# Kernel optimization log

Measured on AMD Instinct MI355X. Metric: run time of the kernel, lower is better.

## Reference

```python
import jax, jax.numpy as jnp
import numpy as np

H = 256          # hidden_dim
E = 2 * H        # encoder output / attention embed dim = 512
MEL = 512        # mel_dim (must equal E for the original attention call to type-check)
NH = 8
HD = E // NH     # 64
B = 16
T = 128
V = 256          # vocab_size
NSPK = 100       # hardcoded speaker embedding rows
MAX_LEN = min(1000, T * 10)  # 1000 decode steps


def setup_inputs() -> dict:
    key = jax.random.key(0)
    ks = iter(jax.random.split(key, 40))

    def w(shape, s=0.05):
        return jax.random.normal(next(ks), shape, dtype=jnp.float32) * s

    return {
        'text_tokens': jax.random.randint(next(ks), (B, T), 0, V),
        'speaker_id': jax.random.randint(next(ks), (B,), 0, NSPK),
        'emb_text': w((V, H)),
        'emb_speaker': w((NSPK, H)),
        # bidirectional encoder LSTM (PyTorch gate order i,f,g,o)
        'enc_f_Wih': w((4 * H, H)), 'enc_f_Whh': w((4 * H, H)),
        'enc_f_bih': w((4 * H,)), 'enc_f_bhh': w((4 * H,)),
        'enc_b_Wih': w((4 * H, H)), 'enc_b_Whh': w((4 * H, H)),
        'enc_b_bih': w((4 * H,)), 'enc_b_bhh': w((4 * H,)),
        # multihead attention in/out projections
        'Wq': w((E, E)), 'bq': w((E,)),
        'Wk': w((E, E)), 'bk': w((E,)),
        'Wv': w((E, E)), 'bv': w((E,)),
        'Wo': w((E, E)), 'bo': w((E,)),
        # decoder LSTM (input dim = E + MEL); hidden state is re-zeroed every
        # step in the original (output state discarded), so Whh never acts.
        'dec_Wih': w((4 * H, E + MEL)), 'dec_Whh': w((4 * H, H)),
        'dec_bih': w((4 * H,)), 'dec_bhh': w((4 * H,)),
        'Wmel': w((MEL, H)), 'bmel': w((MEL,)),
        'Wstop': w((1, H)), 'bstop': w((1,)),
    }


def _lstm(x, Wih, Whh, bih, bhh, reverse=False):
    # x: [B, T, D] -> hidden sequence [B, T, H]
    Bx = x.shape[0]
    Hh = Whh.shape[1]
    h0 = jnp.zeros((Bx, Hh), x.dtype)

    def step(carry, xt):
        h, c = carry
        gates = xt @ Wih.T + bih + h @ Whh.T + bhh
        i, f, g, o = jnp.split(gates, 4, axis=-1)
        c = jax.nn.sigmoid(f) * c + jax.nn.sigmoid(i) * jnp.tanh(g)
        h = jax.nn.sigmoid(o) * jnp.tanh(c)
        return (h, c), h

    _, hs = jax.lax.scan(step, (h0, h0), jnp.swapaxes(x, 0, 1), reverse=reverse)
    return jnp.swapaxes(hs, 0, 1)


def reference(text_tokens, speaker_id, emb_text, emb_speaker,
              enc_f_Wih, enc_f_Whh, enc_f_bih, enc_f_bhh,
              enc_b_Wih, enc_b_Whh, enc_b_bih, enc_b_bhh,
              Wq, bq, Wk, bk, Wv, bv, Wo, bo,
              dec_Wih, dec_Whh, dec_bih, dec_bhh,
              Wmel, bmel, Wstop, bstop):
    # text + speaker embedding
    x = emb_text[text_tokens] + emb_speaker[speaker_id][:, None, :]   # [B,T,H]
    # bidirectional LSTM encoder
    enc_f = _lstm(x, enc_f_Wih, enc_f_Whh, enc_f_bih, enc_f_bhh)
    enc_b = _lstm(x, enc_b_Wih, enc_b_Whh, enc_b_bih, enc_b_bhh, reverse=True)
    enc = jnp.concatenate([enc_f, enc_b], axis=-1)                    # [B,T,E]

    # K/V projections are constant across decode steps -> hoist out of the loop
    K = (enc @ Wk.T + bk).reshape(B, T, NH, HD).transpose(0, 2, 1, 3)   # [B,NH,T,HD]
    Vv = (enc @ Wv.T + bv).reshape(B, T, NH, HD).transpose(0, 2, 1, 3)  # [B,NH,T,HD]
    scale = 1.0 / np.sqrt(HD).astype(np.float32)

    def step(mel_in, _):
        # single-query multihead attention (query = previous mel frame)
        q = (mel_in @ Wq.T + bq).reshape(B, NH, HD)                     # [B,NH,HD]
        w = jax.nn.softmax(jnp.einsum('bhd,bhtd->bht', q, K) * scale, axis=-1)
        ctx = jnp.einsum('bht,bhtd->bhd', w, Vv).reshape(B, E)
        attended = ctx @ Wo.T + bo                                      # [B,E]
        xin = jnp.concatenate([attended, mel_in], axis=-1)              # [B,E+MEL]
        # decoder LSTM single step from ZERO state each step (state discarded
        # in the original), so Whh term vanishes
        gates = xin @ dec_Wih.T + dec_bih + dec_bhh
        i, f, g, o = jnp.split(gates, 4, axis=-1)
        c = jax.nn.sigmoid(i) * jnp.tanh(g)
        h = jax.nn.sigmoid(o) * jnp.tanh(c)                             # [B,H]
        mel = h @ Wmel.T + bmel                                         # [B,MEL]
        stop = h @ Wstop.T + bstop                                      # [B,1]
        return mel, (mel, stop, w.mean(axis=1))

    mel0 = jnp.zeros((B, MEL), jnp.float32)
    _, (mels, stops, attns) = jax.lax.scan(step, mel0, None, length=MAX_LEN)

    mel_output = jnp.swapaxes(mels, 0, 1)    # [B,MAX_LEN,MEL]
    stop_output = jnp.swapaxes(stops, 0, 1)  # [B,MAX_LEN,1]
    attn_last = attns[-1][:, None, :]        # [B,1,T] (head-averaged, last step)
    return mel_output, stop_output, attn_last
```

## Files before the change

kernel.cpp:

```cpp
#include <hip/hip_runtime.h>
#include <hip/hip_bf16.h>


typedef unsigned short u16;
typedef unsigned int   u32;
#define DI __device__ __forceinline__

static constexpr size_t WS_BAR   = 0;
static constexpr size_t WS_GBUF  = 64*1024;
static constexpr size_t WS_HBUF  = 192*1024;
static constexpr size_t WS_PROBS = 208*1024;
static constexpr size_t WS_BIAS  = 272*1024;
static constexpr size_t WS_W2M   = 320*1024;
static constexpr size_t WS_WQH   = 832*1024;
static constexpr size_t WS_WCG   = 1344*1024;

static constexpr size_t OF_ENC_A = 262144;
static constexpr size_t OF_ENC_B = 1286144;
static constexpr size_t OF_XWF   = 4015744;
static constexpr size_t OF_XWB   = 6112896;

DI float bf2f(u16 u){ union{u32 i; float f;} v; v.i = ((u32)u)<<16; return v.f; }
DI u16 f2bf(float f){ union{float f; u32 i;} v; v.f = f;
  u32 r = v.i + 0x7fffu + ((v.i>>16)&1u); return (u16)(r>>16); }
DI float2 bf2x(u32 u){ union{u32 i; float f;} a,b; a.i = u<<16; b.i = u & 0xffff0000u;
  float2 r; r.x = a.f; r.y = b.f; return r; }
DI float dot8(uint4 wv, float4 a, float4 b){
  float2 w0 = bf2x(wv.x), w1 = bf2x(wv.y), w2 = bf2x(wv.z), w3 = bf2x(wv.w);
  return w0.x*a.x + w0.y*a.y + w1.x*a.z + w1.y*a.w
       + w2.x*b.x + w2.y*b.y + w3.x*b.z + w3.y*b.w;
}
DI float dot8f(float4 wa, float4 wb, float4 a, float4 b){
  return wa.x*a.x + wa.y*a.y + wa.z*a.z + wa.w*a.w
       + wb.x*b.x + wb.y*b.y + wb.z*b.z + wb.w*b.w;
}
DI float sigm(float x){ return 1.f/(1.f + __expf(-x)); }

DI float afload(const float* p){
  return __hip_atomic_load(p, __ATOMIC_RELAXED, __HIP_MEMORY_SCOPE_AGENT);
}
DI void afstore(float* p, float v){
  __hip_atomic_store(p, v, __ATOMIC_RELAXED, __HIP_MEMORY_SCOPE_AGENT);
}
DI void aadd(float* p, float v){
  __hip_atomic_fetch_add(p, v, __ATOMIC_RELAXED, __HIP_MEMORY_SCOPE_AGENT);
}

DI void bar_arrive(int* flags, int myidx, int t){
  __syncthreads();
  if (threadIdx.x == 0){
    __builtin_amdgcn_s_waitcnt(0);
    __hip_atomic_store(flags + myidx*32, t, __ATOMIC_RELAXED, __HIP_MEMORY_SCOPE_AGENT);
  }
}
DI void bar_wait(int* flags, int n, int t){
  if (threadIdx.x < 64){
    const int idx = threadIdx.x & (n-1);
    int v = __hip_atomic_load(flags + idx*32, __ATOMIC_RELAXED, __HIP_MEMORY_SCOPE_AGENT);
    while (__any(v < t)){
      __builtin_amdgcn_s_sleep(1);
      if (v < t)
        v = __hip_atomic_load(flags + idx*32, __ATOMIC_RELAXED, __HIP_MEMORY_SCOPE_AGENT);
    }
  }
  __asm__ __volatile__("" ::: "memory");
  __syncthreads();
}

__global__ __launch_bounds__(256) void k_init(int* bars, float* hbuf){
  const int i = blockIdx.x*256 + threadIdx.x;
  for (int k = i; k < 49152; k += 32*256) bars[k] = 0;
  if (i < 4096) hbuf[i] = 0.f;
}

__global__ __launch_bounds__(256) void k_xw(
    const int* __restrict__ tok, const int* __restrict__ spk,
    const float* __restrict__ et, const float* __restrict__ es,
    const float* __restrict__ WihF, const float* __restrict__ bihF, const float* __restrict__ bhhF,
    const float* __restrict__ WihB, const float* __restrict__ bihB, const float* __restrict__ bhhB,
    float* __restrict__ xwf, float* __restrict__ xwb){
  const int tid = threadIdx.x, bi = blockIdx.x;
  const int dir = bi & 1, jc = (bi >> 1) & 3, btg = bi >> 3;
  const int j = jc*256 + tid;
  const float* W = (dir ? WihB : WihF) + j*256;
  const float bias = (dir ? bihB : bihF)[j] + (dir ? bhhB : bhhF)[j];
  float* xw = dir ? xwb : xwf;

  __shared__ __align__(16) float lx[8][256];
  #pragma unroll
  for (int r = 0; r < 8; ++r){
    const int bt = btg*8 + r;
    lx[r][tid] = et[tok[bt]*256 + tid] + es[spk[bt>>7]*256 + tid];
  }
  __syncthreads();

  float acc[8];
  #pragma unroll
  for (int k2 = 0; k2 < 8; ++k2) acc[k2] = bias;
  for (int h = 0; h < 256; h += 8){
    float4 w0 = *(const float4*)(W + h);
    float4 w1 = *(const float4*)(W + h + 4);
    #pragma unroll
    for (int k2 = 0; k2 < 8; ++k2)
      acc[k2] += dot8f(w0, w1, *(const float4*)(&lx[k2][h]), *(const float4*)(&lx[k2][h+4]));
  }
  #pragma unroll
  for (int k2 = 0; k2 < 8; ++k2) xw[(btg*8 + k2)*1024 + j] = acc[k2];
}

__global__ __launch_bounds__(256) void k_fuse(
    const float* __restrict__ decW, const float* __restrict__ Wo,
    const float* __restrict__ Wmel, const float* __restrict__ Wq,
    u16* __restrict__ Wcg, u16* __restrict__ W2m, float* __restrict__ Wqh){
  const int tid = threadIdx.x, blk = blockIdx.x;
  float acc[4] = {0.f,0.f,0.f,0.f};
  if (blk < 512){
    const int g0 = (blk >> 1)*4, e = (blk & 1)*256 + tid;
    for (int jj = 0; jj < 512; ++jj){
      float wo = Wo[jj*512 + e];
      #pragma unroll
      for (int i2 = 0; i2 < 4; ++i2) acc[i2] += decW[(g0+i2)*1024 + jj] * wo;
    }
    #pragma unroll
    for (int i2 = 0; i2 < 4; ++i2) Wcg[(g0+i2)*512 + e] = f2bf(acc[i2]);
  } else if (blk < 768){
    const int g0 = (blk - 512)*4, h = tid;
    for (int m = 0; m < 512; ++m){
      float wm = Wmel[m*256 + h];
      #pragma unroll
      for (int i2 = 0; i2 < 4; ++i2) acc[i2] += decW[(g0+i2)*1024 + 512 + m] * wm;
    }
    #pragma unroll
    for (int i2 = 0; i2 < 4; ++i2) W2m[(g0+i2)*256 + h] = f2bf(acc[i2]);
  } else {
    const int j0 = (blk - 768)*4, h = tid;
    for (int e = 0; e < 512; ++e){
      float wm = Wmel[e*256 + h];
      #pragma unroll
      for (int i2 = 0; i2 < 4; ++i2) acc[i2] += Wq[(j0+i2)*512 + e] * wm;
    }
    #pragma unroll
    for (int i2 = 0; i2 < 4; ++i2) Wqh[(j0+i2)*256 + h] = acc[i2];
  }
}

__global__ __launch_bounds__(256) void k_bias(
    const float* __restrict__ Wq, const float* __restrict__ bq, const float* __restrict__ bmel,
    const float* __restrict__ decW, const float* __restrict__ bo,
    const float* __restrict__ bih, const float* __restrict__ bhh, float* __restrict__ biasws){
  const int o = blockIdx.x*256 + threadIdx.x;
  if (o < 512){
    float s = bq[o];
    for (int e = 0; e < 512; ++e) s += Wq[o*512 + e] * bmel[e];
    biasws[o] = s;
  } else {
    const int gr = o - 512;
    float s1 = bih[gr] + bhh[gr];
    for (int jj = 0; jj < 512; ++jj) s1 += decW[gr*1024 + jj] * bo[jj];
    biasws[512 + gr] = s1;
    float s2 = s1;
    for (int m = 0; m < 512; ++m) s2 += decW[gr*1024 + 512 + m] * bmel[m];
    biasws[1536 + gr] = s2;
  }
}

__global__ __launch_bounds__(128) void k_enc(
    const float* __restrict__ xwf, const float* __restrict__ xwb,
    const float* __restrict__ WhhF, const float* __restrict__ WhhB,
    float* encA, float* encB, int* bars){
  const int tid = threadIdx.x;
  const int xcd = blockIdx.x & 7, sl = blockIdx.x >> 3;
  const int grp = xcd*4 + (sl >> 3);
  const int w = sl & 7;
  const int dir = grp & 1, b = grp >> 1;
  int* bar = bars + (16 + grp)*1024;
  const float* Whh = dir ? WhhB : WhhF;
  const float* xw = dir ? xwb : xwf;
  float* encb = (b < 8 ? encA : encB) + (size_t)(b & 7)*65536;
  const int q = tid >> 5, ii = tid & 31;
  const int j = q*256 + w*32 + ii;
  const float* wr = Whh + j*256;

  __shared__ __align__(16) float l_h[256];
  __shared__ float l_g[4][32];
  __shared__ float l_c[32];
  if (tid < 32) l_c[tid] = 0.f;
  __syncthreads();

  for (int it = 0; it < 128; ++it){
    const int ts = dir ? (127 - it) : it;
    float acc = xw[(b*128 + ts)*1024 + j];
    if (it > 0){
      const int tp = dir ? (ts + 1) : (ts - 1);
      const float* hp = encb + tp*512 + dir*256;
      for (int i = tid; i < 256; i += 128) l_h[i] = afload(hp + i);
      __syncthreads();
      #pragma unroll 4
      for (int k = 0; k < 256; k += 8)
        acc += dot8f(*(const float4*)(wr + k), *(const float4*)(wr + k + 4),
                     *(const float4*)(&l_h[k]), *(const float4*)(&l_h[k + 4]));
    }
    l_g[q][ii] = acc;
    __syncthreads();
    if (tid < 32){
      float ig = l_g[0][tid], fg = l_g[1][tid], gg = l_g[2][tid], og = l_g[3][tid];
      float c = sigm(fg)*l_c[tid] + sigm(ig)*tanhf(gg);
      l_c[tid] = c;
      afstore(encb + ts*512 + dir*256 + w*32 + tid, sigm(og)*tanhf(c));
    }
    bar_arrive(bar, w, it+1);
    bar_wait(bar, 8, it+1);
  }
}

__global__ __launch_bounds__(256) void k_proj(
    const float* __restrict__ encA, const float* __restrict__ encB,
    const float* __restrict__ Wk, const float* __restrict__ bk,
    const float* __restrict__ Wv, const float* __restrict__ bv,
    float* outf){
  const int tid = threadIdx.x, x = blockIdx.x;
  const int role = x & 1, dc = (x >> 1) & 1, btg = x >> 2;
  const int row = dc*256 + tid;
  const float* W = (role ? Wv : Wk) + row*512;
  const float bias = (role ? bv : bk)[row];
  const int b = (btg*8) >> 7;
  const float* eb = (b < 8 ? encA : encB) + (size_t)(b & 7)*65536;
  float acc[8];
  #pragma unroll
  for (int k2 = 0; k2 < 8; ++k2) acc[k2] = bias;
  for (int e = 0; e < 512; e += 8){
    float4 wa = *(const float4*)(W + e);
    float4 wb = *(const float4*)(W + e + 4);
    #pragma unroll
    for (int k2 = 0; k2 < 8; ++k2){
      const float* ep = eb + ((btg*8 + k2) & 127)*512 + e;
      acc[k2] += dot8f(wa, wb, *(const float4*)(ep), *(const float4*)(ep + 4));
    }
  }
  const int head = row >> 6, dd = row & 63;
  float* kv = outf + (size_t)(b >> 1)*1024000 + (size_t)(b & 1)*131072;
  #pragma unroll
  for (int k2 = 0; k2 < 8; ++k2){
    const int ts = (btg*8 + k2) & 127;
    if (role == 0) kv[head*8192 + ts*64 + dd] = acc[k2];
    else           kv[65536 + head*8192 + dd*128 + ts] = acc[k2];
  }
}

__global__ __launch_bounds__(512) void k_decode(
    const float* __restrict__ Wqh,
    const u16*   __restrict__ Wcg,
    const u16*   __restrict__ W2m,
    const float* __restrict__ Wmel,
    const float* __restrict__ bmel,
    const float* __restrict__ Wstop, const float* __restrict__ bstop,
    const float* __restrict__ bq,
    const float* __restrict__ biasws,
    float* Gbuf,
    float* probs, int* bars,
    float* out){
  const int tid = threadIdx.x;
  const int b = blockIdx.x & 15, sidx = blockIdx.x >> 4;
  const int h = sidx >> 1, half = sidx & 1;
  const int d = tid & 63, ko = tid >> 6;
  int* bflag = bars + b*512;
  float* out_mel  = out;
  float* out_stop = out + 8192000;
  float* out_attn = out + 8208000;

  __shared__ __align__(16) float lK[128*68];
  __shared__ __align__(16) float lV[64*132];
  __shared__ __align__(16) float l_h[256];
  __shared__ __align__(16) float l_hw[8*36];
  __shared__ __align__(16) float l_q[64];
  __shared__ __align__(16) float l_p[128];
  __shared__ __align__(16) float l_ct[64];
  __shared__ __align__(16) float l_qt[8][64];
  __shared__ float l_r[2];

  const float* kv = out + (size_t)(b >> 1)*1024000 + (size_t)(b & 1)*131072;
  const int rg = tid >> 2, c4 = tid & 3;
  const int rw = tid >> 3, c8 = tid & 7;
  const int r2 = half*384 + h*48 + rw;

  {
    const float* gK = kv + h*8192;
    for (int i = tid; i < 2048; i += 512){
      const int r = i >> 4, c = i & 15;
      *(float4*)(lK + r*68 + c*4) = *(const float4*)(gK + r*64 + c*4);
    }
    const float* gV = kv + 65536 + h*8192;
    for (int i = tid; i < 2048; i += 512){
      const int r = i >> 5, c = i & 31;
      *(float4*)(lV + r*132 + c*4) = *(const float4*)(gV + r*128 + c*4);
    }
  }

  float4 wq[8];
  {
    const float* p = Wqh + (h*64 + d)*256 + ko*32;
    #pragma unroll
    for (int j = 0; j < 8; ++j) wq[j] = *(const float4*)(p + 4*j);
  }
  uint4 wcg[3][2];
  #pragma unroll
  for (int s = 0; s < 3; ++s){
    const int r = half*384 + rg*3 + s;
    const int orig = r + (r >= 256 ? 256 : 0);
    const u16* p = Wcg + orig*512 + h*64 + c4*16;
    wcg[s][0] = *(const uint4*)(p);
    wcg[s][1] = *(const uint4*)(p + 8);
  }
  uint4 w2[4];
  {
    const int orig2 = r2 + (r2 >= 256 ? 256 : 0);
    const u16* p = W2m + (tid < 384 ? orig2*256 + c8*32 : 0);
    #pragma unroll
    for (int j = 0; j < 4; ++j) w2[j] = *(const uint4*)(p + 8*j);
  }
  const float bq0 = bq[h*64 + d];
  const float bq1 = biasws[h*64 + d];
  const float bmd = bmel[h*64 + half*32 + ((tid & 255) >> 3)];
  float bgi0=0, bgg0=0, bgo0=0, bgi1=0, bgg1=0, bgo1=0;
  if (tid < 256){
    bgi0 = biasws[ 512 + tid]; bgg0 = biasws[1024 + tid]; bgo0 = biasws[1280 + tid];
    bgi1 = biasws[1536 + tid]; bgg1 = biasws[2048 + tid]; bgo1 = biasws[2304 + tid];
  }
  float4 wst4 = {0.f,0.f,0.f,0.f};
  if (h == 0 && half == 1 && tid < 64) wst4 = *(const float4*)(Wstop + tid*4);
  const float bst = bstop[0];

  if (tid < 256) l_h[tid] = 0.f;
  if (tid < 288) l_hw[tid] = 0.f;
  float hreg = 0.f;
  __syncthreads();

  int rot = 0;
  for (int t = 0; t < 1000; ++t){
    float* buf = Gbuf + (rot*16 + b)*768;
    {
      const float4* hh = (const float4*)(l_h + ko*32);
      l_qt[ko][d] = dot8f(wq[0], wq[1], hh[0], hh[1]) + dot8f(wq[2], wq[3], hh[2], hh[3])
                  + dot8f(wq[4], wq[5], hh[4], hh[5]) + dot8f(wq[6], wq[7], hh[6], hh[7]);
    }
    if (tid < 384){
      const float4* hh = (const float4*)(l_hw + c8*36);
      float w2p = dot8(w2[0], hh[0], hh[1]) + dot8(w2[1], hh[2], hh[3])
                + dot8(w2[2], hh[4], hh[5]) + dot8(w2[3], hh[6], hh[7]);
      w2p += __shfl_xor(w2p, 1);
      w2p += __shfl_xor(w2p, 2);
      w2p += __shfl_xor(w2p, 4);
      if (c8 == 0) aadd(buf + r2, w2p);
    } else if (t >= 2 && tid >= 432 && tid < 480){
      int rr = rot + 1; if (rr == 3) rr = 0;
      afstore(Gbuf + (rr*16 + b)*768 + sidx*48 + (tid - 432), 0.f);
    }
    __syncthreads();
    if (tid < 64){
      float qq = (t == 0 ? bq0 : bq1);
      #pragma unroll
      for (int k = 0; k < 8; ++k) qq += l_qt[k][tid];
      l_q[tid] = qq;
      __asm__ __volatile__("s_waitcnt lgkmcnt(0)" ::: "memory");
      const float* kr0 = lK + tid*68;
      const float* kr1 = lK + (tid + 64)*68;
      float s0 = 0.f, s1 = 0.f;
      #pragma unroll
      for (int k = 0; k < 64; k += 8){
        float4 qa = *(const float4*)(l_q + k), qb = *(const float4*)(l_q + k + 4);
        s0 += dot8f(*(const float4*)(kr0 + k), *(const float4*)(kr0 + k + 4), qa, qb);
        s1 += dot8f(*(const float4*)(kr1 + k), *(const float4*)(kr1 + k + 4), qa, qb);
      }
      s0 *= 0.125f; s1 *= 0.125f;
      float m = fmaxf(s0, s1);
      #pragma unroll
      for (int off = 32; off; off >>= 1) m = fmaxf(m, __shfl_xor(m, off));
      float p0 = __expf(s0 - m), p1 = __expf(s1 - m);
      float ss = p0 + p1;
      #pragma unroll
      for (int off = 32; off; off >>= 1) ss += __shfl_xor(ss, off);
      l_p[tid] = p0; l_p[tid + 64] = p1;
      __asm__ __volatile__("s_waitcnt lgkmcnt(0)" ::: "memory");
      const float* vr = lV + tid*132;
      float cs = 0.f;
      #pragma unroll
      for (int k = 0; k < 128; k += 8)
        cs += dot8f(*(const float4*)(vr + k), *(const float4*)(vr + k + 4),
                    *(const float4*)(l_p + k), *(const float4*)(l_p + k + 4));
      l_ct[tid] = cs / ss;
      if (tid == 0) l_r[0] = ss;
    }
    __syncthreads();
    {
      const float4* ct = (const float4*)(l_ct + c4*16);
      float4 c0 = ct[0], c1 = ct[1], c2 = ct[2], c3 = ct[3];
      float pr0 = dot8(wcg[0][0], c0, c1) + dot8(wcg[0][1], c2, c3);
      float pr1 = dot8(wcg[1][0], c0, c1) + dot8(wcg[1][1], c2, c3);
      float pr2 = dot8(wcg[2][0], c0, c1) + dot8(wcg[2][1], c2, c3);
      pr0 += __shfl_xor(pr0, 1); pr0 += __shfl_xor(pr0, 2);
      pr1 += __shfl_xor(pr1, 1); pr1 += __shfl_xor(pr1, 2);
      pr2 += __shfl_xor(pr2, 1); pr2 += __shfl_xor(pr2, 2);
      if (c4 == 0){
        const int rb = half*384 + rg*3;
        aadd(buf + rb,     pr0);
        aadd(buf + rb + 1, pr1);
        aadd(buf + rb + 2, pr2);
      }
    }
    bar_arrive(bflag, sidx, t+1);
    if (t == 1) bar_wait(bars + (b ^ 1)*512, 16, 1);
    if (t > 0){
      if (tid < 256){
        const int dd = half*32 + (tid >> 3), cc = tid & 7;
        const float* pm = Wmel + (h*64 + dd)*256 + cc*32;
        const float4* hh = (const float4*)(l_hw + cc*36);
        float mp = dot8f(*(const float4*)(pm),      *(const float4*)(pm + 4),  hh[0], hh[1])
                 + dot8f(*(const float4*)(pm + 8),  *(const float4*)(pm + 12), hh[2], hh[3])
                 + dot8f(*(const float4*)(pm + 16), *(const float4*)(pm + 20), hh[4], hh[5])
                 + dot8f(*(const float4*)(pm + 24), *(const float4*)(pm + 28), hh[6], hh[7]);
        mp += __shfl_xor(mp, 1); mp += __shfl_xor(mp, 2); mp += __shfl_xor(mp, 4);
        if (cc == 0) out_mel[((size_t)b*1000 + (t-1))*512 + h*64 + dd] = mp + bmd;
      }
      if (h == 0 && half == 1 && tid < 64){
        const float4 h4v = *(const float4*)(l_h + tid*4);
        float sp = wst4.x*h4v.x + wst4.y*h4v.y + wst4.z*h4v.z + wst4.w*h4v.w;
        #pragma unroll
        for (int off = 32; off; off >>= 1) sp += __shfl_xor(sp, off);
        if (tid == 0) out_stop[b*1000 + (t-1)] = sp + bst;
      }
    }
    bar_wait(bflag, 16, t+1);
    if (tid < 256){
      float gi = (t == 0 ? bgi0 : bgi1) + afload(buf + tid);
      float gg = (t == 0 ? bgg0 : bgg1) + afload(buf + 256 + tid);
      float go = (t == 0 ? bgo0 : bgo1) + afload(buf + 512 + tid);
      float c = sigm(gi) * tanhf(gg);
      hreg = sigm(go) * tanhf(c);
      l_h[tid] = hreg;
      l_hw[(tid >> 5)*36 + (tid & 31)] = hreg;
    }
    __syncthreads();
    rot = (rot == 2) ? 0 : rot + 1;
  }

  if (tid < 256){
    const int dd = half*32 + (tid >> 3), cc = tid & 7;
    const float* pm = Wmel + (h*64 + dd)*256 + cc*32;
    const float4* hh = (const float4*)(l_hw + cc*36);
    float mp = dot8f(*(const float4*)(pm),      *(const float4*)(pm + 4),  hh[0], hh[1])
             + dot8f(*(const float4*)(pm + 8),  *(const float4*)(pm + 12), hh[2], hh[3])
             + dot8f(*(const float4*)(pm + 16), *(const float4*)(pm + 20), hh[4], hh[5])
             + dot8f(*(const float4*)(pm + 24), *(const float4*)(pm + 28), hh[6], hh[7]);
    mp += __shfl_xor(mp, 1); mp += __shfl_xor(mp, 2); mp += __shfl_xor(mp, 4);
    if (cc == 0) out_mel[((size_t)b*1000 + 999)*512 + h*64 + dd] = mp + bmd;
  }
  if (h == 0 && half == 1 && tid < 64){
    const float4 h4v = *(const float4*)(l_h + tid*4);
    float sp = wst4.x*h4v.x + wst4.y*h4v.y + wst4.z*h4v.z + wst4.w*h4v.w;
    #pragma unroll
    for (int off = 32; off; off >>= 1) sp += __shfl_xor(sp, off);
    if (tid == 0) out_stop[b*1000 + 999] = sp + bst;
  }
  if (half == 0 && tid < 128)
    afstore(probs + (b*8 + h)*128 + tid, l_p[tid] / l_r[0]);
  bar_arrive(bflag, sidx, 1001);
  if (h == 0 && half == 0){
    bar_wait(bflag, 16, 1001);
    if (tid < 128){
      float ssum = 0.f;
      #pragma unroll
      for (int hh = 0; hh < 8; ++hh) ssum += afload(probs + (b*8 + hh)*128 + tid);
      out_attn[b*128 + tid] = ssum * 0.125f;
    }
  }
}

extern "C" void kernel_launch(void* const* d_in, const int* in_sizes, int n_in,
                              void* d_out, int out_size, void* d_ws, size_t ws_size,
                              hipStream_t stream){
  const int*   tok = (const int*)d_in[0];
  const int*   spk = (const int*)d_in[1];
  const float* emb_text = (const float*)d_in[2];
  const float* emb_spk  = (const float*)d_in[3];
  const float* WihF = (const float*)d_in[4];
  const float* WhhF = (const float*)d_in[5];
  const float* bihF = (const float*)d_in[6];
  const float* bhhF = (const float*)d_in[7];
  const float* WihB = (const float*)d_in[8];
  const float* WhhB = (const float*)d_in[9];
  const float* bihB = (const float*)d_in[10];
  const float* bhhB = (const float*)d_in[11];
  const float* Wq = (const float*)d_in[12];
  const float* bq = (const float*)d_in[13];
  const float* Wk = (const float*)d_in[14];
  const float* bk = (const float*)d_in[15];
  const float* Wv = (const float*)d_in[16];
  const float* bv = (const float*)d_in[17];
  const float* Wo = (const float*)d_in[18];
  const float* bo = (const float*)d_in[19];
  const float* decW = (const float*)d_in[20];
  const float* bih = (const float*)d_in[22];
  const float* bhh = (const float*)d_in[23];
  const float* Wmel = (const float*)d_in[24];
  const float* bmel = (const float*)d_in[25];
  const float* Wstop = (const float*)d_in[26];
  const float* bstop = (const float*)d_in[27];

  char* ws = (char*)d_ws;
  int*   bars   = (int*)(ws + WS_BAR);
  float* Gbuf   = (float*)(ws + WS_GBUF);
  float* hbuf   = (float*)(ws + WS_HBUF);
  float* probs  = (float*)(ws + WS_PROBS);
  float* biasws = (float*)(ws + WS_BIAS);
  u16*   W2m    = (u16*)(ws + WS_W2M);
  float* Wqh    = (float*)(ws + WS_WQH);
  u16*   Wcg    = (u16*)(ws + WS_WCG);

  float* outf = (float*)d_out;
  float* encA = outf + OF_ENC_A;
  float* encB = outf + OF_ENC_B;
  float* xwf  = outf + OF_XWF;
  float* xwb  = outf + OF_XWB;

  k_init <<<32,   256, 0, stream>>>(bars, hbuf);
  k_xw   <<<2048, 256, 0, stream>>>(tok, spk, emb_text, emb_spk,
                                    WihF, bihF, bhhF, WihB, bihB, bhhB, xwf, xwb);
  k_enc  <<<256,  128, 0, stream>>>(xwf, xwb, WhhF, WhhB, encA, encB, bars);
  k_fuse <<<896,  256, 0, stream>>>(decW, Wo, Wmel, Wq, Wcg, W2m, Wqh);
  k_bias <<<6,    256, 0, stream>>>(Wq, bq, bmel, decW, bo, bih, bhh, biasws);
  k_proj <<<1024, 256, 0, stream>>>(encA, encB, Wk, bk, Wv, bv, outf);
  k_decode<<<256, 512, 0, stream>>>(Wqh, Wcg, W2m, Wmel, bmel, Wstop, bstop,
                                    bq, biasws, Gbuf, probs, bars, outf);
}
```

Measured before the change: 6.617 ms.

## Interleave two batch elements per decode block to hide barrier latency

Each decode block now handles two batch elements (b0 and b0+8) with separate shared K/V, hidden and prob buffers, so the grid is halved to 128 blocks. Within each timestep the block does one element's work while the cross-block barrier for the other element completes, and the gate/LSTM update is moved to the start of the next step. Weights held in registers are reused across both elements. The cost is doubled shared memory per block, half as many blocks in flight, and twice the serial work per block per step.

New measurement: 12.39 ms. 1.87x slower.

```diff
diff --git a/kernel.cpp b/kernel.cpp
--- a/kernel.cpp
+++ b/kernel.cpp
@@ -260,39 +260,40 @@
     float* probs, int* bars,
     float* out){
   const int tid = threadIdx.x;
-  const int b = blockIdx.x & 15, sidx = blockIdx.x >> 4;
+  const int b0 = blockIdx.x & 7, sidx = blockIdx.x >> 3;
   const int h = sidx >> 1, half = sidx & 1;
   const int d = tid & 63, ko = tid >> 6;
-  int* bflag = bars + b*512;
   float* out_mel  = out;
   float* out_stop = out + 8192000;
   float* out_attn = out + 8208000;
 
-  __shared__ __align__(16) float lK[128*68];
-  __shared__ __align__(16) float lV[64*132];
-  __shared__ __align__(16) float l_h[256];
-  __shared__ __align__(16) float l_hw[8*36];
+  __shared__ __align__(16) float lK[2][128*68];
+  __shared__ __align__(16) float lV[2][64*132];
+  __shared__ __align__(16) float l_h[2][256];
+  __shared__ __align__(16) float l_hw[2][288];
   __shared__ __align__(16) float l_q[64];
-  __shared__ __align__(16) float l_p[128];
+  __shared__ __align__(16) float l_p[2][128];
   __shared__ __align__(16) float l_ct[64];
   __shared__ __align__(16) float l_qt[8][64];
   __shared__ float l_r[2];
 
-  const float* kv = out + (size_t)(b >> 1)*1024000 + (size_t)(b & 1)*131072;
   const int rg = tid >> 2, c4 = tid & 3;
   const int rw = tid >> 3, c8 = tid & 7;
   const int r2 = half*384 + h*48 + rw;
 
-  {
-    const float* gK = kv + h*8192;
+  #pragma unroll
+  for (int s = 0; s < 2; ++s){
+    const int bb = b0 + 8*s;
+    const float* kvs = out + (size_t)(bb >> 1)*1024000 + (size_t)(bb & 1)*131072;
+    const float* gK = kvs + h*8192;
     for (int i = tid; i < 2048; i += 512){
       const int r = i >> 4, c = i & 15;
-      *(float4*)(lK + r*68 + c*4) = *(const float4*)(gK + r*64 + c*4);
-    }
-    const float* gV = kv + 65536 + h*8192;
+      *(float4*)(&lK[s][r*68 + c*4]) = *(const float4*)(gK + r*64 + c*4);
+    }
+    const float* gV = kvs + 65536 + h*8192;
     for (int i = tid; i < 2048; i += 512){
       const int r = i >> 5, c = i & 31;
-      *(float4*)(lV + r*132 + c*4) = *(const float4*)(gV + r*128 + c*4);
+      *(float4*)(&lV[s][r*132 + c*4]) = *(const float4*)(gV + r*128 + c*4);
     }
   }
 
@@ -330,147 +331,187 @@
   if (h == 0 && half == 1 && tid < 64) wst4 = *(const float4*)(Wstop + tid*4);
   const float bst = bstop[0];
 
-  if (tid < 256) l_h[tid] = 0.f;
-  if (tid < 288) l_hw[tid] = 0.f;
-  float hreg = 0.f;
+  if (tid < 256){ l_h[0][tid] = 0.f; l_h[1][tid] = 0.f; }
+  if (tid < 288){ l_hw[0][tid] = 0.f; l_hw[1][tid] = 0.f; }
   __syncthreads();
 
-  int rot = 0;
   for (int t = 0; t < 1000; ++t){
-    float* buf = Gbuf + (rot*16 + b)*768;
-    {
-      const float4* hh = (const float4*)(l_h + ko*32);
-      l_qt[ko][d] = dot8f(wq[0], wq[1], hh[0], hh[1]) + dot8f(wq[2], wq[3], hh[2], hh[3])
-                  + dot8f(wq[4], wq[5], hh[4], hh[5]) + dot8f(wq[6], wq[7], hh[6], hh[7]);
-    }
-    if (tid < 384){
-      const float4* hh = (const float4*)(l_hw + c8*36);
-      float w2p = dot8(w2[0], hh[0], hh[1]) + dot8(w2[1], hh[2], hh[3])
-                + dot8(w2[2], hh[4], hh[5]) + dot8(w2[3], hh[6], hh[7]);
-      w2p += __shfl_xor(w2p, 1);
-      w2p += __shfl_xor(w2p, 2);
-      w2p += __shfl_xor(w2p, 4);
-      if (c8 == 0) aadd(buf + r2, w2p);
-    } else if (t >= 2 && tid >= 432 && tid < 480){
-      int rr = rot + 1; if (rr == 3) rr = 0;
-      afstore(Gbuf + (rr*16 + b)*768 + sidx*48 + (tid - 432), 0.f);
-    }
-    __syncthreads();
-    if (tid < 64){
-      float qq = (t == 0 ? bq0 : bq1);
-      #pragma unroll
-      for (int k = 0; k < 8; ++k) qq += l_qt[k][tid];
-      l_q[tid] = qq;
-      __asm__ __volatile__("s_waitcnt lgkmcnt(0)" ::: "memory");
-      const float* kr0 = lK + tid*68;
-      const float* kr1 = lK + (tid + 64)*68;
-      float s0 = 0.f, s1 = 0.f;
-      #pragma unroll
-      for (int k = 0; k < 64; k += 8){
-        float4 qa = *(const float4*)(l_q + k), qb = *(const float4*)(l_q + k + 4);
-        s0 += dot8f(*(const float4*)(kr0 + k), *(const float4*)(kr0 + k + 4), qa, qb);
-        s1 += dot8f(*(const float4*)(kr1 + k), *(const float4*)(kr1 + k + 4), qa, qb);
-      }
-      s0 *= 0.125f; s1 *= 0.125f;
-      float m = fmaxf(s0, s1);
-      #pragma unroll
-      for (int off = 32; off; off >>= 1) m = fmaxf(m, __shfl_xor(m, off));
-      float p0 = __expf(s0 - m), p1 = __expf(s1 - m);
-      float ss = p0 + p1;
-      #pragma unroll
-      for (int off = 32; off; off >>= 1) ss += __shfl_xor(ss, off);
-      l_p[tid] = p0; l_p[tid + 64] = p1;
-      __asm__ __volatile__("s_waitcnt lgkmcnt(0)" ::: "memory");
-      const float* vr = lV + tid*132;
-      float cs = 0.f;
-      #pragma unroll
-      for (int k = 0; k < 128; k += 8)
-        cs += dot8f(*(const float4*)(vr + k), *(const float4*)(vr + k + 4),
-                    *(const float4*)(l_p + k), *(const float4*)(l_p + k + 4));
-      l_ct[tid] = cs / ss;
-      if (tid == 0) l_r[0] = ss;
-    }
-    __syncthreads();
-    {
-      const float4* ct = (const float4*)(l_ct + c4*16);
-      float4 c0 = ct[0], c1 = ct[1], c2 = ct[2], c3 = ct[3];
-      float pr0 = dot8(wcg[0][0], c0, c1) + dot8(wcg[0][1], c2, c3);
-      float pr1 = dot8(wcg[1][0], c0, c1) + dot8(wcg[1][1], c2, c3);
-      float pr2 = dot8(wcg[2][0], c0, c1) + dot8(wcg[2][1], c2, c3);
-      pr0 += __shfl_xor(pr0, 1); pr0 += __shfl_xor(pr0, 2);
-      pr1 += __shfl_xor(pr1, 1); pr1 += __shfl_xor(pr1, 2);
-      pr2 += __shfl_xor(pr2, 1); pr2 += __shfl_xor(pr2, 2);
-      if (c4 == 0){
-        const int rb = half*384 + rg*3;
-        aadd(buf + rb,     pr0);
-        aadd(buf + rb + 1, pr1);
-        aadd(buf + rb + 2, pr2);
-      }
-    }
-    bar_arrive(bflag, sidx, t+1);
-    if (t == 1) bar_wait(bars + (b ^ 1)*512, 16, 1);
-    if (t > 0){
+    #pragma unroll
+    for (int s = 0; s < 2; ++s){
+      const int bb = b0 + 8*s;
+      int* bflag = bars + bb*512;
+      float* lHs  = l_h[s];
+      float* lHws = l_hw[s];
+      const float* lKs = lK[s];
+      const float* lVs = lV[s];
+      float* lPs = l_p[s];
+      if (t == 2) bar_wait(bars + (bb ^ 1)*512, 16, 1);
+      if (t >= 2){
+        if (tid < 256){
+          const int dd = half*32 + (tid >> 3), cc = tid & 7;
+          const float* pm = Wmel + (h*64 + dd)*256 + cc*32;
+          const float4* hh = (const float4*)(lHws + cc*36);
+          float mp = dot8f(*(const float4*)(pm),      *(const float4*)(pm + 4),  hh[0], hh[1])
+                   + dot8f(*(const float4*)(pm + 8),  *(const float4*)(pm + 12), hh[2], hh[3])
+                   + dot8f(*(const float4*)(pm + 16), *(const float4*)(pm + 20), hh[4], hh[5])
+                   + dot8f(*(const float4*)(pm + 24), *(const float4*)(pm + 28), hh[6], hh[7]);
+          mp += __shfl_xor(mp, 1); mp += __shfl_xor(mp, 2); mp += __shfl_xor(mp, 4);
+          if (cc == 0) out_mel[((size_t)bb*1000 + (t-2))*512 + h*64 + dd] = mp + bmd;
+        }
+        if (h == 0 && half == 1 && tid < 64){
+          const float4 h4v = *(const float4*)(lHs + tid*4);
+          float sp = wst4.x*h4v.x + wst4.y*h4v.y + wst4.z*h4v.z + wst4.w*h4v.w;
+          #pragma unroll
+          for (int off = 32; off; off >>= 1) sp += __shfl_xor(sp, off);
+          if (tid == 0) out_stop[bb*1000 + (t-2)] = sp + bst;
+        }
+      }
+      if (t >= 1){
+        bar_wait(bflag, 16, t);
+        const float* bufP = Gbuf + (((t-1)%3)*16 + bb)*768;
+        if (tid < 256){
+          float gi = (t == 1 ? bgi0 : bgi1) + afload(bufP + tid);
+          float gg = (t == 1 ? bgg0 : bgg1) + afload(bufP + 256 + tid);
+          float go = (t == 1 ? bgo0 : bgo1) + afload(bufP + 512 + tid);
+          float c = sigm(gi) * tanhf(gg);
+          float hv = sigm(go) * tanhf(c);
+          lHs[tid] = hv;
+          lHws[(tid >> 5)*36 + (tid & 31)] = hv;
+        }
+        __syncthreads();
+      }
+      float* buf = Gbuf + ((t%3)*16 + bb)*768;
+      {
+        const float4* hh = (const float4*)(lHs + ko*32);
+        l_qt[ko][d] = dot8f(wq[0], wq[1], hh[0], hh[1]) + dot8f(wq[2], wq[3], hh[2], hh[3])
+                    + dot8f(wq[4], wq[5], hh[4], hh[5]) + dot8f(wq[6], wq[7], hh[6], hh[7]);
+      }
+      if (tid < 384){
+        const float4* hh = (const float4*)(lHws + c8*36);
+        float w2p = dot8(w2[0], hh[0], hh[1]) + dot8(w2[1], hh[2], hh[3])
+                  + dot8(w2[2], hh[4], hh[5]) + dot8(w2[3], hh[6], hh[7]);
+        w2p += __shfl_xor(w2p, 1);
+        w2p += __shfl_xor(w2p, 2);
+        w2p += __shfl_xor(w2p, 4);
+        if (c8 == 0) aadd(buf + r2, w2p);
+      } else if (t >= 2 && tid >= 432 && tid < 480){
+        const int rr = (t+1)%3;
+        afstore(Gbuf + (rr*16 + bb)*768 + sidx*48 + (tid - 432), 0.f);
+      }
+      __syncthreads();
+      if (tid < 64){
+        float qq = (t == 0 ? bq0 : bq1);
+        #pragma unroll
+        for (int k = 0; k < 8; ++k) qq += l_qt[k][tid];
+        l_q[tid] = qq;
+        __asm__ __volatile__("s_waitcnt lgkmcnt(0)" ::: "memory");
+        const float* kr0 = lKs + tid*68;
+        const float* kr1 = lKs + (tid + 64)*68;
+        float s0 = 0.f, s1 = 0.f;
+        #pragma unroll
+        for (int k = 0; k < 64; k += 8){
+          float4 qa = *(const float4*)(l_q + k), qb = *(const float4*)(l_q + k + 4);
+          s0 += dot8f(*(const float4*)(kr0 + k), *(const float4*)(kr0 + k + 4), qa, qb);
+          s1 += dot8f(*(const float4*)(kr1 + k), *(const float4*)(kr1 + k + 4), qa, qb);
+        }
+        s0 *= 0.125f; s1 *= 0.125f;
+        float m = fmaxf(s0, s1);
+        #pragma unroll
+        for (int off = 32; off; off >>= 1) m = fmaxf(m, __shfl_xor(m, off));
+        float p0 = __expf(s0 - m), p1 = __expf(s1 - m);
+        float ss = p0 + p1;
+        #pragma unroll
+        for (int off = 32; off; off >>= 1) ss += __shfl_xor(ss, off);
+        lPs[tid] = p0; lPs[tid + 64] = p1;
+        __asm__ __volatile__("s_waitcnt lgkmcnt(0)" ::: "memory");
+        const float* vr = lVs + tid*132;
+        float cs = 0.f;
+        #pragma unroll
+        for (int k = 0; k < 128; k += 8)
+          cs += dot8f(*(const float4*)(vr + k), *(const float4*)(vr + k + 4),
+                      *(const float4*)(lPs + k), *(const float4*)(lPs + k + 4));
+        l_ct[tid] = cs / ss;
+        if (tid == 0) l_r[s] = ss;
+      }
+      __syncthreads();
+      {
+        const float4* ct = (const float4*)(l_ct + c4*16);
+        float4 c0 = ct[0], c1 = ct[1], c2 = ct[2], c3 = ct[3];
+        float pr0 = dot8(wcg[0][0], c0, c1) + dot8(wcg[0][1], c2, c3);
+        float pr1 = dot8(wcg[1][0], c0, c1) + dot8(wcg[1][1], c2, c3);
+        float pr2 = dot8(wcg[2][0], c0, c1) + dot8(wcg[2][1], c2, c3);
+        pr0 += __shfl_xor(pr0, 1); pr0 += __shfl_xor(pr0, 2);
+        pr1 += __shfl_xor(pr1, 1); pr1 += __shfl_xor(pr1, 2);
+        pr2 += __shfl_xor(pr2, 1); pr2 += __shfl_xor(pr2, 2);
+        if (c4 == 0){
+          const int rb = half*384 + rg*3;
+          aadd(buf + rb,     pr0);
+          aadd(buf + rb + 1, pr1);
+          aadd(buf + rb + 2, pr2);
+        }
+      }
+      bar_arrive(bflag, sidx, t+1);
+    }
+  }
+
+  #pragma unroll
+  for (int s = 0; s < 2; ++s){
+    const int bb = b0 + 8*s;
+    int* bflag = bars + bb*512;
+    float* lHs  = l_h[s];
+    float* lHws = l_hw[s];
+    float* lPs  = l_p[s];
+    #pragma unroll
+    for (int e = 0; e < 2; ++e){
+      const int tm = 998 + e;
+      if (e == 1){
+        bar_wait(bflag, 16, 1000);
+        const float* bufP = Gbuf + ((999%3)*16 + bb)*768;
+        if (tid < 256){
+          float gi = bgi1 + afload(bufP + tid);
+          float gg = bgg1 + afload(bufP + 256 + tid);
+          float go = bgo1 + afload(bufP + 512 + tid);
+          float c = sigm(gi) * tanhf(gg);
+          float hv = sigm(go) * tanhf(c);
+          lHs[tid] = hv;
+          lHws[(tid >> 5)*36 + (tid & 31)] = hv;
+        }
+        __syncthreads();
+      }
       if (tid < 256){
         const int dd = half*32 + (tid >> 3), cc = tid & 7;
         const float* pm = Wmel + (h*64 + dd)*256 + cc*32;
-        const float4* hh = (const float4*)(l_hw + cc*36);
+        const float4* hh = (const float4*)(lHws + cc*36);
         float mp = dot8f(*(const float4*)(pm),      *(const float4*)(pm + 4),  hh[0], hh[1])
                  + dot8f(*(const float4*)(pm + 8),  *(const float4*)(pm + 12), hh[2], hh[3])
                  + dot8f(*(const float4*)(pm + 16), *(const float4*)(pm + 20), hh[4], hh[5])
                  + dot8f(*(const float4*)(pm + 24), *(const float4*)(pm + 28), hh[6], hh[7]);
         mp += __shfl_xor(mp, 1); mp += __shfl_xor(mp, 2); mp += __shfl_xor(mp, 4);
-        if (cc == 0) out_mel[((size_t)b*1000 + (t-1))*512 + h*64 + dd] = mp + bmd;
+        if (cc == 0) out_mel[((size_t)bb*1000 + tm)*512 + h*64 + dd] = mp + bmd;
       }
       if (h == 0 && half == 1 && tid < 64){
-        const float4 h4v = *(const float4*)(l_h + tid*4);
+        const float4 h4v = *(const float4*)(lHs + tid*4);
         float sp = wst4.x*h4v.x + wst4.y*h4v.y + wst4.z*h4v.z + wst4.w*h4v.w;
         #pragma unroll
         for (int off = 32; off; off >>= 1) sp += __shfl_xor(sp, off);
-        if (tid == 0) out_stop[b*1000 + (t-1)] = sp + bst;
-      }
-    }
-    bar_wait(bflag, 16, t+1);
-    if (tid < 256){
-      float gi = (t == 0 ? bgi0 : bgi1) + afload(buf + tid);
-      float gg = (t == 0 ? bgg0 : bgg1) + afload(buf + 256 + tid);
-      float go = (t == 0 ? bgo0 : bgo1) + afload(buf + 512 + tid);
-      float c = sigm(gi) * tanhf(gg);
-      hreg = sigm(go) * tanhf(c);
-      l_h[tid] = hreg;
-      l_hw[(tid >> 5)*36 + (tid & 31)] = hreg;
-    }
-    __syncthreads();
-    rot = (rot == 2) ? 0 : rot + 1;
-  }
-
-  if (tid < 256){
-    const int dd = half*32 + (tid >> 3), cc = tid & 7;
-    const float* pm = Wmel + (h*64 + dd)*256 + cc*32;
-    const float4* hh = (const float4*)(l_hw + cc*36);
-    float mp = dot8f(*(const float4*)(pm),      *(const float4*)(pm + 4),  hh[0], hh[1])
-             + dot8f(*(const float4*)(pm + 8),  *(const float4*)(pm + 12), hh[2], hh[3])
-             + dot8f(*(const float4*)(pm + 16), *(const float4*)(pm + 20), hh[4], hh[5])
-             + dot8f(*(const float4*)(pm + 24), *(const float4*)(pm + 28), hh[6], hh[7]);
-    mp += __shfl_xor(mp, 1); mp += __shfl_xor(mp, 2); mp += __shfl_xor(mp, 4);
-    if (cc == 0) out_mel[((size_t)b*1000 + 999)*512 + h*64 + dd] = mp + bmd;
-  }
-  if (h == 0 && half == 1 && tid < 64){
-    const float4 h4v = *(const float4*)(l_h + tid*4);
-    float sp = wst4.x*h4v.x + wst4.y*h4v.y + wst4.z*h4v.z + wst4.w*h4v.w;
-    #pragma unroll
-    for (int off = 32; off; off >>= 1) sp += __shfl_xor(sp, off);
-    if (tid == 0) out_stop[b*1000 + 999] = sp + bst;
-  }
-  if (half == 0 && tid < 128)
-    afstore(probs + (b*8 + h)*128 + tid, l_p[tid] / l_r[0]);
-  bar_arrive(bflag, sidx, 1001);
-  if (h == 0 && half == 0){
-    bar_wait(bflag, 16, 1001);
-    if (tid < 128){
-      float ssum = 0.f;
-      #pragma unroll
-      for (int hh = 0; hh < 8; ++hh) ssum += afload(probs + (b*8 + hh)*128 + tid);
-      out_attn[b*128 + tid] = ssum * 0.125f;
+        if (tid == 0) out_stop[bb*1000 + tm] = sp + bst;
+      }
+    }
+    if (half == 0 && tid < 128)
+      afstore(probs + (bb*8 + h)*128 + tid, lPs[tid] / l_r[s]);
+    bar_arrive(bflag, sidx, 1001);
+  }
+  #pragma unroll
+  for (int s = 0; s < 2; ++s){
+    const int bb = b0 + 8*s;
+    if (h == 0 && half == 0){
+      bar_wait(bars + bb*512, 16, 1001);
+      if (tid < 128){
+        float ssum = 0.f;
+        #pragma unroll
+        for (int hh = 0; hh < 8; ++hh) ssum += afload(probs + (bb*8 + hh)*128 + tid);
+        out_attn[bb*128 + tid] = ssum * 0.125f;
+      }
     }
   }
 }
@@ -529,6 +570,6 @@
   k_fuse <<<896,  256, 0, stream>>>(decW, Wo, Wmel, Wq, Wcg, W2m, Wqh);
   k_bias <<<6,    256, 0, stream>>>(Wq, bq, bmel, decW, bo, bih, bhh, biasws);
   k_proj <<<1024, 256, 0, stream>>>(encA, encB, Wk, bk, Wv, bv, outf);
-  k_decode<<<256, 512, 0, stream>>>(Wqh, Wcg, W2m, Wmel, bmel, Wstop, bstop,
+  k_decode<<<128, 512, 0, stream>>>(Wqh, Wcg, W2m, Wmel, bmel, Wstop, bstop,
                                     bq, biasws, Gbuf, probs, bars, outf);
 }
```

## Double-buffer decoder hidden state and defer mel projection off the critical path

Applied to the files above, without the earlier changes.

Restructures the decode loop so each step starts by waiting on the barrier and computing h from the gate buffer. The mel/stop projection for step t-2 now runs between the barrier wait and the LSTM nonlinearity, using a double-buffered copy of the previous hidden state. The projection moves off the stretch between bar_arrive and bar_wait, and the loop tail's extra sync is folded into the loop head. It adds an epilogue for the last two steps plus more shared memory, and output writes now lag by two steps.

Measured after the change: 7.458 ms. +12.7%, slower.

```diff
diff --git a/kernel.cpp b/kernel.cpp
--- a/kernel.cpp
+++ b/kernel.cpp
@@ -264,14 +264,15 @@
   const int h = sidx >> 1, half = sidx & 1;
   const int d = tid & 63, ko = tid >> 6;
   int* bflag = bars + b*512;
+  int* pflag = bars + (b ^ 1)*512;
   float* out_mel  = out;
   float* out_stop = out + 8192000;
   float* out_attn = out + 8208000;
 
   __shared__ __align__(16) float lK[128*68];
   __shared__ __align__(16) float lV[64*132];
-  __shared__ __align__(16) float l_h[256];
-  __shared__ __align__(16) float l_hw[8*36];
+  __shared__ __align__(16) float l_h[2][256];
+  __shared__ __align__(16) float l_hw[2][288];
   __shared__ __align__(16) float l_q[64];
   __shared__ __align__(16) float l_p[128];
   __shared__ __align__(16) float l_ct[64];
@@ -330,21 +331,56 @@
   if (h == 0 && half == 1 && tid < 64) wst4 = *(const float4*)(Wstop + tid*4);
   const float bst = bstop[0];
 
-  if (tid < 256) l_h[tid] = 0.f;
-  if (tid < 288) l_hw[tid] = 0.f;
-  float hreg = 0.f;
+  if (tid < 256) l_h[0][tid] = 0.f;
+  if (tid < 288) l_hw[0][tid] = 0.f;
   __syncthreads();
 
-  int rot = 0;
   for (int t = 0; t < 1000; ++t){
-    float* buf = Gbuf + (rot*16 + b)*768;
+    const int cur = t & 1, prv = cur ^ 1;
+    if (t >= 1) bar_wait(bflag, 16, t);
+    if (t == 2) bar_wait(pflag, 16, 1);
+    float gi = 0.f, gg = 0.f, go = 0.f;
+    if (t >= 1 && tid < 256){
+      const float* bp = Gbuf + (((t-1)%3)*16 + b)*768;
+      gi = afload(bp + tid); gg = afload(bp + 256 + tid); go = afload(bp + 512 + tid);
+    }
+    if (t >= 2){
+      if (tid < 256){
+        const int dd = half*32 + (tid >> 3), cc = tid & 7;
+        const float* pm = Wmel + (h*64 + dd)*256 + cc*32;
+        const float4* hh = (const float4*)(&l_hw[prv][cc*36]);
+        float mp = dot8f(*(const float4*)(pm),      *(const float4*)(pm + 4),  hh[0], hh[1])
+                 + dot8f(*(const float4*)(pm + 8),  *(const float4*)(pm + 12), hh[2], hh[3])
+                 + dot8f(*(const float4*)(pm + 16), *(const float4*)(pm + 20), hh[4], hh[5])
+                 + dot8f(*(const float4*)(pm + 24), *(const float4*)(pm + 28), hh[6], hh[7]);
+        mp += __shfl_xor(mp, 1); mp += __shfl_xor(mp, 2); mp += __shfl_xor(mp, 4);
+        if (cc == 0) out_mel[((size_t)b*1000 + (t-2))*512 + h*64 + dd] = mp + bmd;
+      }
+      if (h == 0 && half == 1 && tid < 64){
+        const float4 h4v = *(const float4*)(&l_h[prv][tid*4]);
+        float sp = wst4.x*h4v.x + wst4.y*h4v.y + wst4.z*h4v.z + wst4.w*h4v.w;
+        #pragma unroll
+        for (int off = 32; off; off >>= 1) sp += __shfl_xor(sp, off);
+        if (tid == 0) out_stop[b*1000 + (t-2)] = sp + bst;
+      }
+    }
+    if (t >= 1 && tid < 256){
+      float gI = (t == 1 ? bgi0 : bgi1) + gi;
+      float gG = (t == 1 ? bgg0 : bgg1) + gg;
+      float gO = (t == 1 ? bgo0 : bgo1) + go;
+      float hv = sigm(gO) * tanhf(sigm(gI) * tanhf(gG));
+      l_h[cur][tid] = hv;
+      l_hw[cur][(tid >> 5)*36 + (tid & 31)] = hv;
+    }
+    __syncthreads();
+    float* buf = Gbuf + ((t%3)*16 + b)*768;
     {
-      const float4* hh = (const float4*)(l_h + ko*32);
+      const float4* hh = (const float4*)(&l_h[cur][ko*32]);
       l_qt[ko][d] = dot8f(wq[0], wq[1], hh[0], hh[1]) + dot8f(wq[2], wq[3], hh[2], hh[3])
                   + dot8f(wq[4], wq[5], hh[4], hh[5]) + dot8f(wq[6], wq[7], hh[6], hh[7]);
     }
     if (tid < 384){
-      const float4* hh = (const float4*)(l_hw + c8*36);
+      const float4* hh = (const float4*)(&l_hw[cur][c8*36]);
       float w2p = dot8(w2[0], hh[0], hh[1]) + dot8(w2[1], hh[2], hh[3])
                 + dot8(w2[2], hh[4], hh[5]) + dot8(w2[3], hh[6], hh[7]);
       w2p += __shfl_xor(w2p, 1);
@@ -352,7 +388,7 @@
       w2p += __shfl_xor(w2p, 4);
       if (c8 == 0) aadd(buf + r2, w2p);
     } else if (t >= 2 && tid >= 432 && tid < 480){
-      int rr = rot + 1; if (rr == 3) rr = 0;
+      const int rr = (t+1)%3;
       afstore(Gbuf + (rr*16 + b)*768 + sidx*48 + (tid - 432), 0.f);
     }
     __syncthreads();
@@ -408,45 +444,43 @@
       }
     }
     bar_arrive(bflag, sidx, t+1);
-    if (t == 1) bar_wait(bars + (b ^ 1)*512, 16, 1);
-    if (t > 0){
-      if (tid < 256){
-        const int dd = half*32 + (tid >> 3), cc = tid & 7;
-        const float* pm = Wmel + (h*64 + dd)*256 + cc*32;
-        const float4* hh = (const float4*)(l_hw + cc*36);
-        float mp = dot8f(*(const float4*)(pm),      *(const float4*)(pm + 4),  hh[0], hh[1])
-                 + dot8f(*(const float4*)(pm + 8),  *(const float4*)(pm + 12), hh[2], hh[3])
-                 + dot8f(*(const float4*)(pm + 16), *(const float4*)(pm + 20), hh[4], hh[5])
-                 + dot8f(*(const float4*)(pm + 24), *(const float4*)(pm + 28), hh[6], hh[7]);
-        mp += __shfl_xor(mp, 1); mp += __shfl_xor(mp, 2); mp += __shfl_xor(mp, 4);
-        if (cc == 0) out_mel[((size_t)b*1000 + (t-1))*512 + h*64 + dd] = mp + bmd;
-      }
-      if (h == 0 && half == 1 && tid < 64){
-        const float4 h4v = *(const float4*)(l_h + tid*4);
-        float sp = wst4.x*h4v.x + wst4.y*h4v.y + wst4.z*h4v.z + wst4.w*h4v.w;
-        #pragma unroll
-        for (int off = 32; off; off >>= 1) sp += __shfl_xor(sp, off);
-        if (tid == 0) out_stop[b*1000 + (t-1)] = sp + bst;
-      }
-    }
-    bar_wait(bflag, 16, t+1);
-    if (tid < 256){
-      float gi = (t == 0 ? bgi0 : bgi1) + afload(buf + tid);
-      float gg = (t == 0 ? bgg0 : bgg1) + afload(buf + 256 + tid);
-      float go = (t == 0 ? bgo0 : bgo1) + afload(buf + 512 + tid);
-      float c = sigm(gi) * tanhf(gg);
-      hreg = sigm(go) * tanhf(c);
-      l_h[tid] = hreg;
-      l_hw[(tid >> 5)*36 + (tid & 31)] = hreg;
-    }
-    __syncthreads();
-    rot = (rot == 2) ? 0 : rot + 1;
-  }
-
+  }
+
+  bar_wait(bflag, 16, 1000);
+  float gi = 0.f, gg = 0.f, go = 0.f;
+  if (tid < 256){
+    const float* bp = Gbuf + ((999%3)*16 + b)*768;
+    gi = afload(bp + tid); gg = afload(bp + 256 + tid); go = afload(bp + 512 + tid);
+  }
   if (tid < 256){
     const int dd = half*32 + (tid >> 3), cc = tid & 7;
     const float* pm = Wmel + (h*64 + dd)*256 + cc*32;
-    const float4* hh = (const float4*)(l_hw + cc*36);
+    const float4* hh = (const float4*)(&l_hw[1][cc*36]);
+    float mp = dot8f(*(const float4*)(pm),      *(const float4*)(pm + 4),  hh[0], hh[1])
+             + dot8f(*(const float4*)(pm + 8),  *(const float4*)(pm + 12), hh[2], hh[3])
+             + dot8f(*(const float4*)(pm + 16), *(const float4*)(pm + 20), hh[4], hh[5])
+             + dot8f(*(const float4*)(pm + 24), *(const float4*)(pm + 28), hh[6], hh[7]);
+    mp += __shfl_xor(mp, 1); mp += __shfl_xor(mp, 2); mp += __shfl_xor(mp, 4);
+    if (cc == 0) out_mel[((size_t)b*1000 + 998)*512 + h*64 + dd] = mp + bmd;
+  }
+  if (h == 0 && half == 1 && tid < 64){
+    const float4 h4v = *(const float4*)(&l_h[1][tid*4]);
+    float sp = wst4.x*h4v.x + wst4.y*h4v.y + wst4.z*h4v.z + wst4.w*h4v.w;
+    #pragma unroll
+    for (int off = 32; off; off >>= 1) sp += __shfl_xor(sp, off);
+    if (tid == 0) out_stop[b*1000 + 998] = sp + bst;
+  }
+  if (tid < 256){
+    float gI = bgi1 + gi, gG = bgg1 + gg, gO = bgo1 + go;
+    float hv = sigm(gO) * tanhf(sigm(gI) * tanhf(gG));
+    l_h[0][tid] = hv;
+    l_hw[0][(tid >> 5)*36 + (tid & 31)] = hv;
+  }
+  __syncthreads();
+  if (tid < 256){
+    const int dd = half*32 + (tid >> 3), cc = tid & 7;
+    const float* pm = Wmel + (h*64 + dd)*256 + cc*32;
+    const float4* hh = (const float4*)(&l_hw[0][cc*36]);
     float mp = dot8f(*(const float4*)(pm),      *(const float4*)(pm + 4),  hh[0], hh[1])
              + dot8f(*(const float4*)(pm + 8),  *(const float4*)(pm + 12), hh[2], hh[3])
              + dot8f(*(const float4*)(pm + 16), *(const float4*)(pm + 20), hh[4], hh[5])
@@ -455,7 +489,7 @@
     if (cc == 0) out_mel[((size_t)b*1000 + 999)*512 + h*64 + dd] = mp + bmd;
   }
   if (h == 0 && half == 1 && tid < 64){
-    const float4 h4v = *(const float4*)(l_h + tid*4);
+    const float4 h4v = *(const float4*)(&l_h[0][tid*4]);
     float sp = wst4.x*h4v.x + wst4.y*h4v.y + wst4.z*h4v.z + wst4.w*h4v.w;
     #pragma unroll
     for (int off = 32; off; off >>= 1) sp += __shfl_xor(sp, off);
```
